# Optimization experiments

Measured on AMD Instinct MI355X. Metric: run time of the kernel, lower is better.

## Reference

```python
import jax, jax.numpy as jnp
import numpy as np

B, NS, NI, UP = 1024, 64, 64, 4
H = 256


def setup_inputs() -> dict:
    key = jax.random.key(0)
    ks = list(jax.random.split(key, 40))
    it = iter(ks)
    def lin(din, dout):
        return (jax.random.normal(next(it), (din, dout), jnp.float32) / np.sqrt(din)).astype(jnp.float32)
    d = {}
    d['rays_o'] = jax.random.normal(next(it), (B, 3), jnp.float32) * 0.1
    rd = jax.random.normal(next(it), (B, 3), jnp.float32)
    d['rays_d'] = rd / jnp.linalg.norm(rd, axis=-1, keepdims=True)
    d['near'] = jnp.full((B, 1), 0.5, jnp.float32)
    d['far'] = jnp.full((B, 1), 2.5, jnp.float32)
    d['W_sdf0'] = lin(3, H); d['b_sdf0'] = jnp.zeros((H,), jnp.float32)
    d['W_sdf1'] = lin(H, H); d['b_sdf1'] = jnp.zeros((H,), jnp.float32)
    d['W_sdf2'] = lin(H, 1 + H); d['b_sdf2'] = jnp.zeros((1 + H,), jnp.float32)
    d['s_var'] = jnp.asarray(0.3, jnp.float32)
    d['Wc0'] = lin(9 + H, H); d['bc0'] = jnp.zeros((H,), jnp.float32)
    d['Wc1'] = lin(H, 3); d['bc1'] = jnp.zeros((3,), jnp.float32)
    d['Wn0'] = lin(6, H); d['bn0'] = jnp.zeros((H,), jnp.float32)
    d['Wn1'] = lin(H, H); d['bn1'] = jnp.zeros((H,), jnp.float32)
    d['Wn2'] = lin(H, 4); d['bn2'] = jnp.zeros((4,), jnp.float32)
    d['Wrf0'] = lin(3, H); d['brf0'] = jnp.zeros((H,), jnp.float32)
    d['Wrf1'] = lin(H, 1); d['brf1'] = jnp.zeros((1,), jnp.float32)
    d['Wrl0'] = lin(3, H); d['brl0'] = jnp.zeros((H,), jnp.float32)
    d['Wrl1'] = lin(H, 1); d['brl1'] = jnp.zeros((1,), jnp.float32)
    d['Wnm0'] = lin(H, 128); d['bnm0'] = jnp.zeros((128,), jnp.float32)
    d['Wnm1'] = lin(128, 3); d['bnm1'] = jnp.zeros((3,), jnp.float32)
    return d


def _forward(args):
    (rays_o, rays_d, near, far, W_sdf0, b_sdf0, W_sdf1, b_sdf1, W_sdf2, b_sdf2,
     s_var, Wc0, bc0, Wc1, bc1, Wn0, bn0, Wn1, bn1, Wn2, bn2,
     Wrf0, brf0, Wrf1, brf1, Wrl0, brl0, Wrl1, brl1, Wnm0, bnm0, Wnm1, bnm1) = args
    relu, sig = jax.nn.relu, jax.nn.sigmoid
    Bn = rays_o.shape[0]
    inv_s = jnp.clip(jnp.exp(10.0 * s_var), 1e-6, 1e6)  # SingleVarianceNetwork
    sample_dist = 2.0 / NS

    def sdf_out(p):
        h = relu(p @ W_sdf0 + b_sdf0)
        h = relu(h @ W_sdf1 + b_sdf1)
        return h @ W_sdf2 + b_sdf2  # [N, 1+256]: sdf + feature

    def sdf_val(p):
        return sdf_out(p)[..., 0]

    def sample_pdf(bins, weights, n):  # deterministic (perturb=False)
        w = weights + 1e-5
        pdf = w / jnp.sum(w, -1, keepdims=True)
        cdf = jnp.concatenate([jnp.zeros_like(pdf[:, :1]), jnp.cumsum(pdf, -1)], -1)
        u = jnp.broadcast_to(jnp.linspace(0.5 / n, 1.0 - 0.5 / n, n, dtype=bins.dtype), (bins.shape[0], n))
        inds = jax.vmap(lambda c, uu: jnp.searchsorted(c, uu, side='right'))(cdf, u)
        below = jnp.clip(inds - 1, 0, bins.shape[-1] - 1)
        above = jnp.clip(inds, 0, bins.shape[-1] - 1)
        cb = jnp.take_along_axis(cdf, below, -1); ca = jnp.take_along_axis(cdf, above, -1)
        bb = jnp.take_along_axis(bins, below, -1); ba = jnp.take_along_axis(bins, above, -1)
        denom = jnp.where(ca - cb < 1e-5, 1.0, ca - cb)
        return bb + (u - cb) / denom * (ba - bb)

    def up_sample(o, d, z, sdf, n_imp, s):  # NeuS hierarchical SDF upsampling
        pts = o[:, None, :] + d[:, None, :] * z[..., None]
        radius = jnp.linalg.norm(pts, axis=-1)
        inside = ((radius[:, :-1] < 1.0) | (radius[:, 1:] < 1.0)).astype(z.dtype)
        prev_sdf, next_sdf = sdf[:, :-1], sdf[:, 1:]
        prev_z, next_z = z[:, :-1], z[:, 1:]
        mid_sdf = 0.5 * (prev_sdf + next_sdf)
        cos_val = (next_sdf - prev_sdf) / (next_z - prev_z + 1e-5)
        prev_cos = jnp.concatenate([jnp.zeros_like(cos_val[:, :1]), cos_val[:, :-1]], -1)
        cos_val = jnp.clip(jnp.minimum(cos_val, prev_cos), -1e3, 0.0) * inside
        dist = next_z - prev_z
        pc = sig((mid_sdf - 0.5 * cos_val * dist) * s)
        nc = sig((mid_sdf + 0.5 * cos_val * dist) * s)
        alpha = (pc - nc + 1e-5) / (pc + 1e-5)
        trans = jnp.cumprod(jnp.concatenate([jnp.ones_like(alpha[:, :1]), 1.0 - alpha + 1e-7], -1), -1)[:, :-1]
        return sample_pdf(z, alpha * trans, n_imp)

    def importance_sdf(o, d):
        z = near + (far - near) * jnp.linspace(0.0, 1.0, NS)[None, :]
        sdf = sdf_val((o[:, None, :] + d[:, None, :] * z[..., None]).reshape(-1, 3)).reshape(Bn, -1)
        for i in range(UP):
            nz = up_sample(o, d, z, sdf, NI // UP, 64.0 * 2 ** i)
            z = jnp.sort(jnp.concatenate([z, nz], -1), -1)
            if i + 1 < UP:
                sdf = sdf_val((o[:, None, :] + d[:, None, :] * z[..., None]).reshape(-1, 3)).reshape(Bn, -1)
        return jax.lax.stop_gradient(z)  # sampler runs under no_grad

    def render_sdf(o, d, z):  # rendering_rays_SDF (NeuS)
        S = z.shape[1]
        dists = jnp.concatenate([z[:, 1:] - z[:, :-1], jnp.full_like(z[:, :1], sample_dist)], -1)
        mid_z = z + 0.5 * dists
        pts = (o[:, None, :] + d[:, None, :] * mid_z[..., None]).reshape(-1, 3)
        dirs = jnp.broadcast_to(d[:, None, :], (Bn, S, 3)).reshape(-1, 3)
        out = sdf_out(pts)
        sdf = out[:, :1]; feat = out[:, 1:]
        grads = jax.grad(lambda p: jnp.sum(sdf_val(p)))(pts)  # analytic SDF gradient
        true_cos = jnp.sum(dirs * grads, -1, keepdims=True)
        iter_cos = -relu(-true_cos)  # cos_anneal_ratio = 1.0
        df = dists.reshape(-1, 1)
        pc = sig((sdf - 0.5 * iter_cos * df) * inv_s)
        nc = sig((sdf + 0.5 * iter_cos * df) * inv_s)
        alpha = jnp.clip((pc - nc + 1e-5) / (pc + 1e-5), 0.0, 1.0).reshape(Bn, S)
        trans = jnp.cumprod(jnp.concatenate([jnp.ones_like(alpha[:, :1]), 1.0 - alpha + 1e-7], -1), -1)[:, :-1]
        w = alpha * trans
        depths = jax.lax.stop_gradient(jnp.sum(mid_z * w, -1, keepdims=True))  # AlphaBlend depth, no_grad
        nrm = grads / (jnp.linalg.norm(grads, axis=-1, keepdims=True) + 1e-12)  # NormalizedAnalytic
        cin = jnp.concatenate([pts, nrm, dirs, feat], -1)  # color_d_in=9 + 256 feat
        rgb = sig(relu(cin @ Wc0 + bc0) @ Wc1 + bc1).reshape(Bn, S, 3)
        color = jnp.sum(rgb * w[..., None], 1)
        smooth = ((feat @ Wnm0 + bnm0) @ Wnm1 + bnm1).reshape(Bn, S, 3)  # Linear->Linear, no act
        surf_n = jnp.sum(w[..., None] * nrm.reshape(Bn, S, 3), 1)
        surf_n = surf_n / (jnp.linalg.norm(surf_n, axis=-1, keepdims=True) + 1e-12)
        return color, w, depths, surf_n, smooth

    def nerf_eval(pts, dirs):
        h = relu(jnp.concatenate([pts, dirs], -1) @ Wn0 + bn0)
        h = relu(h @ Wn1 + bn1)
        o = h @ Wn2 + bn2
        return o[:, 0], sig(o[:, 1:4])

    def mask_prob(pts, Wa, ba, Wb, bb):  # Refract/ReflectNetwork, d_in=3 d_out=1
        return sig((relu(pts @ Wa + ba) @ Wb + bb)[:, 0])

    def importance_nerf(o, d, z, n_imp):
        S = z.shape[1]
        dists = jnp.concatenate([z[:, 1:] - z[:, :-1], jnp.full_like(z[:, :1], 1e10)], -1)
        pts = (o[:, None, :] + d[:, None, :] * z[..., None]).reshape(-1, 3)
        dirs = jnp.broadcast_to(d[:, None, :], (Bn, S, 3)).reshape(-1, 3)
        sigma, _ = nerf_eval(pts, dirs)
        alpha = 1.0 - jnp.exp(-relu(sigma).reshape(Bn, S) * dists)
        trans = jnp.cumprod(jnp.concatenate([jnp.ones_like(alpha[:, :1]), 1.0 - alpha + 1e-7], -1), -1)[:, :-1]
        w = alpha * trans
        nz = sample_pdf(z, w[:, :-1], n_imp)
        return jax.lax.stop_gradient(jnp.sort(jnp.concatenate([z, nz], -1), -1))

    def render_nerf(o, d, z):
        S = z.shape[1]
        dists = jnp.concatenate([z[:, 1:] - z[:, :-1], jnp.full_like(z[:, :1], sample_dist)], -1)
        mid_z = z + 0.5 * dists
        pts = (o[:, None, :] + d[:, None, :] * mid_z[..., None]).reshape(-1, 3)
        dirs = jnp.broadcast_to(d[:, None, :], (Bn, S, 3)).reshape(-1, 3)
        sigma, rgb = nerf_eval(pts, dirs)
        alpha = 1.0 - jnp.exp(-relu(sigma).reshape(Bn, S) * dists)
        trans = jnp.cumprod(jnp.concatenate([jnp.ones_like(alpha[:, :1]), 1.0 - alpha + 1e-7], -1), -1)[:, :-1]
        w = alpha * trans
        color = jnp.sum(rgb.reshape(Bn, S, 3) * w[..., None], 1)
        m1 = jnp.sum(w * mask_prob(pts, Wrf0, brf0, Wrf1, brf1).reshape(Bn, S), -1, keepdims=True)
        m2 = jnp.sum(w * mask_prob(pts, Wrl0, brl0, Wrl1, brl1).reshape(Bn, S), -1, keepdims=True)
        return color, m1, m2

    # ---- main pipeline (eval: perturb=False, geometry_warmup_state=False) ----
    z_sdf = importance_sdf(rays_o, rays_d)
    _color_sdf, _w_sdf, depths, surf_n, _smooth = render_sdf(rays_o, rays_d, z_sdf)

    z0 = near + (far - near) * jnp.linspace(0.0, 1.0, NS)[None, :]
    z1 = importance_nerf(rays_o, rays_d, z0, NI)
    c1, m1, m2 = render_nerf(rays_o, rays_d, z1)

    # hit point + reflect/refract directions
    hit = rays_o + rays_d * depths
    n = surf_n
    cos = jnp.sum(rays_d * n, -1, keepdims=True)
    n = jnp.where(cos > 0, -n, n)  # face the incoming ray
    cosi = -jnp.sum(rays_d * n, -1, keepdims=True)
    refl = rays_d + 2.0 * cosi * n
    eta = 1.0 / 1.5
    k = 1.0 - eta * eta * (1.0 - cosi * cosi)
    refr = eta * rays_d + (eta * cosi - jnp.sqrt(jnp.maximum(k, 0.0))) * n
    refr = jnp.where(k < 0, refl, refr)  # total internal reflection
    refl = refl / (jnp.linalg.norm(refl, axis=-1, keepdims=True) + 1e-12)
    refr = refr / (jnp.linalg.norm(refr, axis=-1, keepdims=True) + 1e-12)

    ones = jnp.ones((Bn, 1), z1.dtype)
    # reflect (fanshe) pass: near=0.05 far=3.7
    zf0 = 0.05 * ones + (3.7 - 0.05) * jnp.linspace(0.0, 1.0, NS)[None, :]
    zf = importance_nerf(hit, refl, zf0, NI)
    cf, _, _ = render_nerf(hit, refl, zf)
    # refract (zheshe) passes: (0,3.7) and (0.5,3.7) with half samples
    zz0 = 3.7 * jnp.linspace(0.0, 1.0, NS // 2)[None, :] * ones
    zz = importance_nerf(hit, refr, zz0, NI // 2)
    cz, _, _ = render_nerf(hit, refr, zz)
    zb0 = 0.5 * ones + (3.7 - 0.5) * jnp.linspace(0.0, 1.0, NS // 2)[None, :]
    zb = importance_nerf(hit, refr, zb0, NI // 2)
    cb_, _, _ = render_nerf(hit, refr, zb)
    rgb_z = 0.5 * cz + 0.5 * cb_

    rgb = c1 * (1.0 - m2) + cf * m2
    rgb = rgb * (1.0 - m1) + rgb_z * m1
    return rgb


def reference(rays_o, rays_d, near, far, W_sdf0, b_sdf0, W_sdf1, b_sdf1, W_sdf2, b_sdf2,
              s_var, Wc0, bc0, Wc1, bc1, Wn0, bn0, Wn1, bn1, Wn2, bn2,
              Wrf0, brf0, Wrf1, brf1, Wrl0, brl0, Wrl1, brl1, Wnm0, bnm0, Wnm1, bnm1):
    return _forward((rays_o, rays_d, near, far, W_sdf0, b_sdf0, W_sdf1, b_sdf1, W_sdf2, b_sdf2,
                     s_var, Wc0, bc0, Wc1, bc1, Wn0, bn0, Wn1, bn1, Wn2, bn2,
                     Wrf0, brf0, Wrf1, brf1, Wrl0, brl0, Wrl1, brl1, Wnm0, bnm0, Wnm1, bnm1))
```

## Files before the change

### kernel.cpp

```cpp
#include <hip/hip_runtime.h>

#define NB 1024
#define HH 256
#define ZS 128
#define PP 16
#define SAMPLE_DIST 0.03125f

typedef __attribute__((ext_vector_type(8))) _Float16 half8v;
typedef __attribute__((ext_vector_type(4))) float f32x4;

struct ZInit { int on; const float* loA; const float* hiA; float lo0,hi0,lo1,hi1; };

__device__ __forceinline__ float sigm(float x){ return 1.0f/(1.0f+__expf(-x)); }

__device__ __forceinline__ void gload_lds16(const void* g, void* l){
  __builtin_amdgcn_global_load_lds(
      (const __attribute__((address_space(1))) unsigned int*)g,
      (__attribute__((address_space(3))) unsigned int*)l, 16, 0, 0);
}

__device__ __forceinline__ float iscan_prod(float v, int lane){
  #pragma unroll
  for (int o=1;o<64;o<<=1){ float u=__shfl_up(v,o); if(lane>=o) v*=u; }
  return v;
}
__device__ __forceinline__ float iscan_sum(float v, int lane){
  #pragma unroll
  for (int o=1;o<64;o<<=1){ float u=__shfl_up(v,o); if(lane>=o) v+=u; }
  return v;
}
__device__ __forceinline__ float wave_sum(float v){
  #pragma unroll
  for (int o=1;o<64;o<<=1) v += __shfl_xor(v,o);
  return v;
}

__device__ __forceinline__ void load_point2(const float* __restrict__ o, const float* __restrict__ dv,
    const float* __restrict__ z, int idx, int S, int midflag, int zst, ZInit zi, float* pt, float* dir)
{
  int r = idx / S;
  int i = idx - r*S;
  float zz;
  if (zi.on){
    float a=zi.loA[r], b=zi.hiA[r];
    zz = a + (b-a)*((float)i/(float)(S-1));
    if (midflag){
      float z1 = a + (b-a)*((float)(i+1)/(float)(S-1));
      zz = (i < S-1) ? 0.5f*(zz+z1) : (zz + 0.5f*SAMPLE_DIST);
    }
  } else {
    const float* zr = z + r*zst;
    zz = zr[i];
    if (midflag) zz = (i < S-1) ? 0.5f*(zz + zr[i+1]) : (zz + 0.5f*SAMPLE_DIST);
  }
  #pragma unroll
  for (int c=0;c<3;c++){
    float dc = dv[r*3+c];
    pt[c] = o[r*3+c] + dc*zz;
    if (dir) dir[c] = dc;
  }
}

__device__ __forceinline__ void load_point(const float* __restrict__ o, const float* __restrict__ dv,
    const float* __restrict__ z, int idx, int S, int midflag, float* pt, float* dir)
{
  int r = idx / S;
  int i = idx - r*S;
  const float* zr = z + r*ZS;
  float zz = zr[i];
  if (midflag) zz = (i < S-1) ? 0.5f*(zz + zr[i+1]) : (zz + 0.5f*SAMPLE_DIST);
  #pragma unroll
  for (int c=0;c<3;c++){
    float dc = dv[r*3+c];
    pt[c] = o[r*3+c] + dc*zz;
    if (dir) dir[c] = dc;
  }
}

__global__ __launch_bounds__(256) void prep_kernel(const float* __restrict__ W1, const float* __restrict__ W2,
    float* __restrict__ W1T, float* __restrict__ w2col)
{
  int idx = blockIdx.x*256 + threadIdx.x;
  int j = idx >> 8, k = idx & 255;
  W1T[j*HH + k] = W1[k*HH + j];
  if (idx < HH) w2col[idx] = W2[idx*257];
}

__global__ __launch_bounds__(256) void prep_bfrag_kernel(const float* __restrict__ W1,
    short* __restrict__ Bh)
{
  int idx = blockIdx.x*256 + threadIdx.x;
  int j = idx & 7;
  int lane = (idx>>3) & 63;
  int s = (idx>>9) & 7;
  int nt = idx >> 12;
  int k = s*32 + ((lane>>4)<<3) + j;
  int n = nt*16 + (lane&15);
  union { _Float16 h; short s; } u;
  u.h = (_Float16)W1[k*256 + n];
  Bh[idx] = u.s;
}

__global__ void build_rays_kernel(const float* __restrict__ ro, const float* __restrict__ rd,
    const float* __restrict__ nearA, const float* __restrict__ farA,
    const float* __restrict__ hit, const float* __restrict__ refl, const float* __restrict__ refr,
    float* __restrict__ rO, float* __restrict__ rD, float* __restrict__ rLo, float* __restrict__ rHi)
{
  int r = blockIdx.x*256 + threadIdx.x;
  if (r >= 4096) return;
  int m = r>>10, q = r&1023;
  const float* so; const float* sd; float lo,hi;
  if (m==0){ so=ro+q*3; sd=rd+q*3; lo=nearA[q]; hi=farA[q]; }
  else if (m==1){ so=hit+q*3; sd=refl+q*3; lo=0.05f; hi=3.7f; }
  else if (m==2){ so=hit+q*3; sd=refr+q*3; lo=0.f; hi=3.7f; }
  else { so=hit+q*3; sd=refr+q*3; lo=0.5f; hi=3.7f; }
  rO[r*3]=so[0]; rO[r*3+1]=so[1]; rO[r*3+2]=so[2];
  rD[r*3]=sd[0]; rD[r*3+1]=sd[1]; rD[r*3+2]=sd[2];
  rLo[r]=lo; rHi[r]=hi;
}

__global__ __launch_bounds__(256) void sdf_mfma_kernel(
    const float* __restrict__ o, const float* __restrict__ dv, const float* __restrict__ z,
    int S, int midflag, int zst, ZInit zi,
    const float* __restrict__ W0, const float* __restrict__ b0,
    const short* __restrict__ Bh, const float* __restrict__ b1,
    const float* __restrict__ w2col, const float* __restrict__ b2,
    float* __restrict__ out_sdf, unsigned short* __restrict__ signs)
{
  __shared__ short ldsB[2][8192];
  __shared__ float xs[128][5];
  __shared__ float w0s[3*HH];
  __shared__ float b0s[HH];
  int t = threadIdx.x;
  int base = blockIdx.x*128;
  int wave=t>>6, lane=t&63, g=lane>>4, c16=lane&15;
  for (int i=t;i<3*HH;i+=256) w0s[i]=W0[i];
  b0s[t]=b0[t];
  if (t<128){
    float pt[3];
    load_point2(o,dv,z,base+t,S,midflag,zst,zi,pt,nullptr);
    xs[t][0]=pt[0]; xs[t][1]=pt[1]; xs[t][2]=pt[2];
  }
  {
    const char* gb = (const char*)Bh;
    #pragma unroll
    for (int c=0;c<4;c++){
      int ch = wave*4 + c;
      gload_lds16(gb + ch*1024 + lane*16, (void*)&ldsB[0][ch*512]);
    }
  }
  __syncthreads();
  half8v af[2][8];
  #pragma unroll
  for (int mt=0;mt<2;mt++){
    const float* xp = xs[wave*32 + mt*16 + c16];
    float x0=xp[0],x1=xp[1],x2=xp[2];
    #pragma unroll
    for (int s8=0;s8<8;s8++){
      int nb = s8*32 + g*8;
      union { _Float16 h[8]; half8v v; } uh;
      #pragma unroll
      for (int j=0;j<8;j++){
        int n=nb+j;
        float a=b0s[n];
        a=fmaf(x0,w0s[n],a);
        a=fmaf(x1,w0s[HH+n],a);
        a=fmaf(x2,w0s[2*HH+n],a);
        uh.h[j]=(_Float16)fmaxf(a,0.f);
      }
      af[mt][s8]=uh.v;
    }
  }
  float pacc[2][4];
  #pragma unroll
  for (int mt=0;mt<2;mt++){ pacc[mt][0]=0.f; pacc[mt][1]=0.f; pacc[mt][2]=0.f; pacc[mt][3]=0.f; }
  int buf=0;
  for (int ntp=0;ntp<8;ntp++){
    if (ntp<7){
      const char* gb = (const char*)(Bh + 2*(ntp+1)*4096);
      #pragma unroll
      for (int c=0;c<4;c++){
        int ch = wave*4 + c;
        gload_lds16(gb + ch*1024 + lane*16, (void*)&ldsB[buf^1][ch*512]);
      }
    }
    int nt0=2*ntp;
    f32x4 aH[2][2];
    #pragma unroll
    for (int mt=0;mt<2;mt++)
      #pragma unroll
      for (int h=0;h<2;h++) aH[mt][h]=(f32x4){0.f,0.f,0.f,0.f};
    const short* Lb = &ldsB[buf][0];
    #pragma unroll
    for (int s8=0;s8<8;s8++){
      half8v bh0 = *(const half8v*)(Lb + s8*512 + lane*8);
      half8v bh1 = *(const half8v*)(Lb + 4096 + s8*512 + lane*8);
      #pragma unroll
      for (int mt=0;mt<2;mt++){
        aH[mt][0] = __builtin_amdgcn_mfma_f32_16x16x32_f16(af[mt][s8], bh0, aH[mt][0], 0,0,0);
        aH[mt][1] = __builtin_amdgcn_mfma_f32_16x16x32_f16(af[mt][s8], bh1, aH[mt][1], 0,0,0);
      }
    }
    #pragma unroll
    for (int h=0;h<2;h++){
      int nt = nt0+h;
      int n = nt*16 + c16;
      float b1v = b1[n];
      float wv = w2col[n];
      #pragma unroll
      for (int mt=0;mt<2;mt++){
        f32x4 acc = aH[mt][h];
        #pragma unroll
        for (int rr=0;rr<4;rr++){
          float hv = acc[rr]+b1v;
          if (signs){
            unsigned long long m0 = __ballot(hv>0.f);
            if (c16==0) signs[(base+wave*32+mt*16+g*4+rr)*16+nt] = (unsigned short)(m0>>(16*g));
          }
          pacc[mt][rr]=fmaf(fmaxf(hv,0.f),wv,pacc[mt][rr]);
        }
      }
    }
    __syncthreads();
    buf^=1;
  }
  #pragma unroll
  for (int mt=0;mt<2;mt++)
    #pragma unroll
    for (int rr=0;rr<4;rr++){
      float v=pacc[mt][rr];
      v+=__shfl_xor(v,1); v+=__shfl_xor(v,2); v+=__shfl_xor(v,4); v+=__shfl_xor(v,8);
      pacc[mt][rr]=v;
    }
  if (c16==0){
    float bb2=b2[0];
    #pragma unroll
    for (int mt=0;mt<2;mt++)
      #pragma unroll
      for (int rr=0;rr<4;rr++)
        out_sdf[base + wave*32 + mt*16 + g*4 + rr] = pacc[mt][rr] + bb2;
  }
}

__global__ __launch_bounds__(256) void sdf_bwd_mfma_kernel(
    const float* __restrict__ o, const float* __restrict__ dv, const float* __restrict__ z,
    const float* __restrict__ W0, const float* __restrict__ b0,
    const unsigned short* __restrict__ signs,
    const short* __restrict__ Th,
    const float* __restrict__ w2col,
    float* __restrict__ out_grad)
{
  __shared__ short ldsB[2][8192];
  __shared__ float xs[128][5];
  __shared__ float w0s[3*HH];
  __shared__ float b0s[HH];
  __shared__ _Float16 w2h_s[HH];
  int t = threadIdx.x;
  int base = blockIdx.x*128;
  int wave=t>>6, lane=t&63, g=lane>>4, c16=lane&15;
  for (int i=t;i<3*HH;i+=256) w0s[i]=W0[i];
  b0s[t]=b0[t];
  w2h_s[t]=(_Float16)w2col[t];
  if (t<128){
    float pt[3];
    ZInit zn{0,nullptr,nullptr,0,0,0,0};
    load_point2(o,dv,z,base+t,128,1,ZS,zn,pt,nullptr);
    xs[t][0]=pt[0]; xs[t][1]=pt[1]; xs[t][2]=pt[2];
  }
  {
    const char* gb = (const char*)Th;
    #pragma unroll
    for (int c=0;c<4;c++){
      int ch = wave*4 + c;
      gload_lds16(gb + ch*1024 + lane*16, (void*)&ldsB[0][ch*512]);
    }
  }
  __syncthreads();
  half8v af[2][8];
  #pragma unroll
  for (int mt=0;mt<2;mt++){
    int ptA = base + wave*32 + mt*16 + c16;
    #pragma unroll
    for (int s8=0;s8<8;s8++){
      int j0 = s8*32 + g*8;
      unsigned short wch = signs[ptA*16 + (j0>>4)];
      unsigned bits = ((unsigned)wch >> ((g&1)*8)) & 0xFFu;
      union { _Float16 h[8]; half8v v; } uh;
      #pragma unroll
      for (int jj=0;jj<8;jj++){
        bool on = (bits>>jj)&1u;
        uh.h[jj] = on ? w2h_s[j0+jj] : (_Float16)0.f;
      }
      af[mt][s8]=uh.v;
    }
  }
  float acc3[2][4][3];
  #pragma unroll
  for (int mt=0;mt<2;mt++)
    #pragma unroll
    for (int rr=0;rr<4;rr++){ acc3[mt][rr][0]=0.f; acc3[mt][rr][1]=0.f; acc3[mt][rr][2]=0.f; }
  int buf=0;
  for (int ntp=0;ntp<8;ntp++){
    if (ntp<7){
      const char* gb = (const char*)(Th + 2*(ntp+1)*4096);
      #pragma unroll
      for (int c=0;c<4;c++){
        int ch = wave*4 + c;
        gload_lds16(gb + ch*1024 + lane*16, (void*)&ldsB[buf^1][ch*512]);
      }
    }
    int nt0=2*ntp;
    f32x4 aH[2][2];
    #pragma unroll
    for (int mt=0;mt<2;mt++)
      #pragma unroll
      for (int h=0;h<2;h++) aH[mt][h]=(f32x4){0.f,0.f,0.f,0.f};
    const short* Lb = &ldsB[buf][0];
    #pragma unroll
    for (int s8=0;s8<8;s8++){
      half8v bh0 = *(const half8v*)(Lb + s8*512 + lane*8);
      half8v bh1 = *(const half8v*)(Lb + 4096 + s8*512 + lane*8);
      #pragma unroll
      for (int mt=0;mt<2;mt++){
        aH[mt][0] = __builtin_amdgcn_mfma_f32_16x16x32_f16(af[mt][s8], bh0, aH[mt][0], 0,0,0);
        aH[mt][1] = __builtin_amdgcn_mfma_f32_16x16x32_f16(af[mt][s8], bh1, aH[mt][1], 0,0,0);
      }
    }
    #pragma unroll
    for (int h=0;h<2;h++){
      int nt = nt0+h;
      int tn = nt*16 + c16;
      float w0a=w0s[tn], w0b=w0s[HH+tn], w0c=w0s[2*HH+tn], bb=b0s[tn];
      #pragma unroll
      for (int mt=0;mt<2;mt++){
        f32x4 acc = aH[mt][h];
        #pragma unroll
        for (int rr=0;rr<4;rr++){
          const float* xq = xs[wave*32 + mt*16 + g*4 + rr];
          float h0 = fmaf(xq[0],w0a, fmaf(xq[1],w0b, fmaf(xq[2],w0c, bb)));
          float dh0 = (h0>0.f) ? acc[rr] : 0.f;
          acc3[mt][rr][0]=fmaf(dh0,w0a,acc3[mt][rr][0]);
          acc3[mt][rr][1]=fmaf(dh0,w0b,acc3[mt][rr][1]);
          acc3[mt][rr][2]=fmaf(dh0,w0c,acc3[mt][rr][2]);
        }
      }
    }
    __syncthreads();
    buf^=1;
  }
  #pragma unroll
  for (int mt=0;mt<2;mt++)
    #pragma unroll
    for (int rr=0;rr<4;rr++)
      #pragma unroll
      for (int cc=0;cc<3;cc++){
        float v=acc3[mt][rr][cc];
        v+=__shfl_xor(v,1); v+=__shfl_xor(v,2); v+=__shfl_xor(v,4); v+=__shfl_xor(v,8);
        acc3[mt][rr][cc]=v;
      }
  if (c16==0){
    #pragma unroll
    for (int mt=0;mt<2;mt++)
      #pragma unroll
      for (int rr=0;rr<4;rr++){
        int pt_ = base + wave*32 + mt*16 + g*4 + rr;
        out_grad[pt_*3+0]=acc3[mt][rr][0];
        out_grad[pt_*3+1]=acc3[mt][rr][1];
        out_grad[pt_*3+2]=acc3[mt][rr][2];
      }
  }
}

__global__ __launch_bounds__(256) void nerf_mfma_batch(
    const float* __restrict__ rO, const float* __restrict__ rD,
    const float* __restrict__ rLo, const float* __restrict__ rHi,
    const float* __restrict__ zbuf, int ptsA, int lgSA, int lgSB, int NRA, int useZ, int midflag,
    const float* __restrict__ W0, const float* __restrict__ b0,
    const short* __restrict__ Bh, const float* __restrict__ b1,
    const float* __restrict__ W2, const float* __restrict__ b2,
    float* __restrict__ out_sigma, float* __restrict__ out_rgb)
{
  __shared__ short ldsB[2][8192];
  __shared__ float w0s[6*HH];
  __shared__ float b0s[HH];
  int t = threadIdx.x;
  int base = blockIdx.x*128;
  int wave=t>>6, lane=t&63, g=lane>>4, c16=lane&15;
  for (int i=t;i<6*HH;i+=256) w0s[i]=W0[i];
  b0s[t]=b0[t];
  {
    const char* gb = (const char*)Bh;
    #pragma unroll
    for (int c=0;c<4;c++){
      int ch = wave*4 + c;
      gload_lds16(gb + ch*1024 + lane*16, (void*)&ldsB[0][ch*512]);
    }
  }
  float xv[2][6];
  #pragma unroll
  for (int mt=0;mt<2;mt++){
    int idx = base + wave*32 + mt*16 + c16;
    int r,i,S;
    if (idx<ptsA){ r=idx>>lgSA; i=idx-(r<<lgSA); S=1<<lgSA; }
    else { int q=idx-ptsA; int rq=q>>lgSB; r=NRA+rq; i=q-(rq<<lgSB); S=1<<lgSB; }
    float zz;
    if (!useZ){
      float a=rLo[r], b=rHi[r];
      zz = a + (b-a)*((float)i/(float)(S-1));
      if (midflag){
        float z1 = a + (b-a)*((float)(i+1)/(float)(S-1));
        zz = (i<S-1)? 0.5f*(zz+z1) : (zz+0.5f*SAMPLE_DIST);
      }
    } else {
      const float* zr = zbuf + r*128;
      zz = zr[i];
      if (midflag) zz = (i<S-1)? 0.5f*(zz+zr[i+1]) : (zz+0.5f*SAMPLE_DIST);
    }
    #pragma unroll
    for (int c=0;c<3;c++){
      float dc=rD[r*3+c];
      xv[mt][c]   = rO[r*3+c] + dc*zz;
      xv[mt][3+c] = dc;
    }
  }
  __syncthreads();
  half8v af[2][8];
  #pragma unroll
  for (int mt=0;mt<2;mt++){
    float x0=xv[mt][0],x1=xv[mt][1],x2=xv[mt][2],x3=xv[mt][3],x4=xv[mt][4],x5=xv[mt][5];
    #pragma unroll
    for (int s8=0;s8<8;s8++){
      int nb = s8*32 + g*8;
      union { _Float16 h[8]; half8v v; } uh;
      #pragma unroll
      for (int j=0;j<8;j++){
        int n=nb+j;
        float a=b0s[n];
        a=fmaf(x0,w0s[n],a);
        a=fmaf(x1,w0s[HH+n],a);
        a=fmaf(x2,w0s[2*HH+n],a);
        a=fmaf(x3,w0s[3*HH+n],a);
        a=fmaf(x4,w0s[4*HH+n],a);
        a=fmaf(x5,w0s[5*HH+n],a);
        uh.h[j]=(_Float16)fmaxf(a,0.f);
      }
      af[mt][s8]=uh.v;
    }
  }
  float pacc[2][4][4];
  #pragma unroll
  for (int mt=0;mt<2;mt++)
    #pragma unroll
    for (int rr=0;rr<4;rr++){ pacc[mt][rr][0]=0.f; pacc[mt][rr][1]=0.f; pacc[mt][rr][2]=0.f; pacc[mt][rr][3]=0.f; }
  int buf=0;
  for (int ntp=0;ntp<8;ntp++){
    if (ntp<7){
      const char* gb = (const char*)(Bh + 2*(ntp+1)*4096);
      #pragma unroll
      for (int c=0;c<4;c++){
        int ch = wave*4 + c;
        gload_lds16(gb + ch*1024 + lane*16, (void*)&ldsB[buf^1][ch*512]);
      }
    }
    int nt0=2*ntp;
    f32x4 aH[2][2];
    #pragma unroll
    for (int mt=0;mt<2;mt++)
      #pragma unroll
      for (int h=0;h<2;h++) aH[mt][h]=(f32x4){0.f,0.f,0.f,0.f};
    const short* Lb = &ldsB[buf][0];
    #pragma unroll
    for (int s8=0;s8<8;s8++){
      half8v bh0 = *(const half8v*)(Lb + s8*512 + lane*8);
      half8v bh1 = *(const half8v*)(Lb + 4096 + s8*512 + lane*8);
      #pragma unroll
      for (int mt=0;mt<2;mt++){
        aH[mt][0] = __builtin_amdgcn_mfma_f32_16x16x32_f16(af[mt][s8], bh0, aH[mt][0], 0,0,0);
        aH[mt][1] = __builtin_amdgcn_mfma_f32_16x16x32_f16(af[mt][s8], bh1, aH[mt][1], 0,0,0);
      }
    }
    #pragma unroll
    for (int h=0;h<2;h++){
      int nt = nt0+h;
      int n = nt*16 + c16;
      float b1v = b1[n];
      float4 w2v = *(const float4*)(W2 + n*4);
      #pragma unroll
      for (int mt=0;mt<2;mt++){
        f32x4 acc = aH[mt][h];
        #pragma unroll
        for (int rr=0;rr<4;rr++){
          float hh = fmaxf(acc[rr]+b1v, 0.f);
          pacc[mt][rr][0]=fmaf(hh,w2v.x,pacc[mt][rr][0]);
          pacc[mt][rr][1]=fmaf(hh,w2v.y,pacc[mt][rr][1]);
          pacc[mt][rr][2]=fmaf(hh,w2v.z,pacc[mt][rr][2]);
          pacc[mt][rr][3]=fmaf(hh,w2v.w,pacc[mt][rr][3]);
        }
      }
    }
    __syncthreads();
    buf^=1;
  }
  #pragma unroll
  for (int mt=0;mt<2;mt++)
    #pragma unroll
    for (int rr=0;rr<4;rr++)
      #pragma unroll
      for (int c=0;c<4;c++){
        float v=pacc[mt][rr][c];
        v+=__shfl_xor(v,1); v+=__shfl_xor(v,2); v+=__shfl_xor(v,4); v+=__shfl_xor(v,8);
        pacc[mt][rr][c]=v;
      }
  if (c16==0){
    float bb0=b2[0], bb1=b2[1], bb2v=b2[2], bb3=b2[3];
    #pragma unroll
    for (int mt=0;mt<2;mt++)
      #pragma unroll
      for (int rr=0;rr<4;rr++){
        int pt_ = base + wave*32 + mt*16 + g*4 + rr;
        out_sigma[pt_] = pacc[mt][rr][0] + bb0;
        out_rgb[pt_*3+0] = sigm(pacc[mt][rr][1] + bb1);
        out_rgb[pt_*3+1] = sigm(pacc[mt][rr][2] + bb2v);
        out_rgb[pt_*3+2] = sigm(pacc[mt][rr][3] + bb3);
      }
  }
}

__global__ __launch_bounds__(256) void mask_kernel(
    const float* __restrict__ o, const float* __restrict__ dv, const float* __restrict__ z, int S,
    const float* __restrict__ Wa0, const float* __restrict__ ba0, const float* __restrict__ Wa1, const float* __restrict__ ba1,
    const float* __restrict__ Wb0, const float* __restrict__ bb0, const float* __restrict__ Wb1, const float* __restrict__ bb1,
    float* __restrict__ outA, float* __restrict__ outB)
{
  __shared__ __align__(16) float hA[PP][HH];
  __shared__ float pin[PP][4];
  __shared__ float part[PP][16];
  int t=threadIdx.x;
  int base=blockIdx.x*PP;
  if (t<PP){
    float pt[3];
    load_point(o,dv,z,base+t,S,1,pt,nullptr);
    pin[t][0]=pt[0]; pin[t][1]=pt[1]; pin[t][2]=pt[2];
  }
  __syncthreads();
  {
    float w0=Wa0[t], w1=Wa0[HH+t], w2=Wa0[2*HH+t], bb=ba0[t];
    #pragma unroll
    for (int p=0;p<PP;p++){
      float v = fmaf(pin[p][0],w0, fmaf(pin[p][1],w1, fmaf(pin[p][2],w2, bb)));
      hA[p][t]=fmaxf(v,0.f);
    }
  }
  __syncthreads();
  {
    int p=t>>4, g=t&15;
    float s=0.f;
    #pragma unroll
    for (int m=0;m<16;m++){ int j=g+16*m; s=fmaf(hA[p][j], Wa1[j], s); }
    part[p][g]=s;
  }
  __syncthreads();
  if (t<PP){
    float s=ba1[0];
    #pragma unroll
    for (int g=0;g<16;g++) s+=part[t][g];
    outA[base+t]=sigm(s);
  }
  __syncthreads();
  {
    float w0=Wb0[t], w1=Wb0[HH+t], w2=Wb0[2*HH+t], bb=bb0[t];
    #pragma unroll
    for (int p=0;p<PP;p++){
      float v = fmaf(pin[p][0],w0, fmaf(pin[p][1],w1, fmaf(pin[p][2],w2, bb)));
      hA[p][t]=fmaxf(v,0.f);
    }
  }
  __syncthreads();
  {
    int p=t>>4, g=t&15;
    float s=0.f;
    #pragma unroll
    for (int m=0;m<16;m++){ int j=g+16*m; s=fmaf(hA[p][j], Wb1[j], s); }
    part[p][g]=s;
  }
  __syncthreads();
  if (t<PP){
    float s=bb1[0];
    #pragma unroll
    for (int g=0;g<16;g++) s+=part[t][g];
    outB[base+t]=sigm(s);
  }
}

__global__ __launch_bounds__(256) void upsample_wave_kernel(float* __restrict__ z,
    const float* __restrict__ sdf, const float* __restrict__ o, const float* __restrict__ dv,
    int S, float s, ZInit zi)
{
  __shared__ float zsh[4][128], ssh[4][128], csh[4][128], nzsh[4][16];
  int wave=threadIdx.x>>6, lane=threadIdx.x&63;
  int r=blockIdx.x*4+wave;
  float* zs=zsh[wave]; float* ss=ssh[wave]; float* cs=csh[wave]; float* nzs=nzsh[wave];
  for (int i=lane;i<S;i+=64){
    float zv;
    if (zi.on){
      float a=zi.loA[r], b=zi.hiA[r];
      zv = a + (b-a)*((float)i/(float)(S-1));
    } else zv = z[r*ZS+i];
    zs[i]=zv; ss[i]=sdf[r*S+i];
  }
  __syncthreads();
  float ox=o[r*3],oy=o[r*3+1],oz=o[r*3+2];
  float dx=dv[r*3],dy=dv[r*3+1],dz=dv[r*3+2];
  int M=S-1;
  auto alpha_at=[&](int k)->float{
    float z0=zs[k], z1=zs[k+1], s0=ss[k], s1=ss[k+1];
    float craw=(s1-s0)/(z1-z0+1e-5f);
    float cprev=(k>0)? (ss[k]-ss[k-1])/(zs[k]-zs[k-1]+1e-5f) : 0.f;
    float cv=fminf(craw,cprev);
    cv=fminf(fmaxf(cv,-1000.f),0.f);
    float px=ox+dx*z0, py=oy+dy*z0, pz=oz+dz*z0;
    float qx=ox+dx*z1, qy=oy+dy*z1, qz=oz+dz*z1;
    float r0=sqrtf(px*px+py*py+pz*pz);
    float r1=sqrtf(qx*qx+qy*qy+qz*qz);
    float inside=(r0<1.f||r1<1.f)?1.f:0.f;
    cv*=inside;
    float mid=0.5f*(s0+s1), dist=z1-z0;
    float pc=sigm((mid-0.5f*cv*dist)*s);
    float nc=sigm((mid+0.5f*cv*dist)*s);
    return (pc-nc+1e-5f)/(pc+1e-5f);
  };
  float al0=(lane<M)? alpha_at(lane):0.f;
  float al1=(lane+64<M)? alpha_at(lane+64):0.f;
  float f0=(lane<M)?(1.f-al0+1e-7f):1.f;
  float f1=(lane+64<M)?(1.f-al1+1e-7f):1.f;
  float ip0=iscan_prod(f0,lane);
  float tt=__shfl_up(ip0,1); float T0=(lane==0)?1.f:tt;
  float tot0=__shfl(ip0,63);
  float ip1=iscan_prod(f1,lane);
  float tu=__shfl_up(ip1,1); float T1=((lane==0)?1.f:tu)*tot0;
  float w0=(lane<M)? al0*T0+1e-5f:0.f;
  float w1=(lane+64<M)? al1*T1+1e-5f:0.f;
  float wsum=wave_sum(w0+w1);
  float inv=1.f/wsum;
  float is0=iscan_sum(w0,lane);
  float st0=__shfl(is0,63);
  float is1=iscan_sum(w1,lane)+st0;
  if (lane<M) cs[lane+1]=is0*inv;
  if (lane+64<M) cs[lane+64+1]=is1*inv;
  if (lane==0) cs[0]=0.f;
  __syncthreads();
  if (lane<16){
    float u=(lane+0.5f)/16.f;
    int lo=0,hi=S;
    while(lo<hi){ int m=(lo+hi)>>1; if(cs[m]<=u) lo=m+1; else hi=m; }
    int below=lo-1; below=below<0?0:(below>S-1?S-1:below);
    int above=lo>S-1?S-1:lo;
    float cb=cs[below], ca=cs[above], bb=zs[below], ba=zs[above];
    float dd=ca-cb; float den=(dd<1e-5f)?1.f:dd;
    nzs[lane]=bb+(u-cb)/den*(ba-bb);
  }
  __syncthreads();
  for (int i=lane;i<S;i+=64){
    float zi_=zs[i]; int cnt=0;
    #pragma unroll
    for (int j=0;j<16;j++) cnt += (nzs[j]<zi_)?1:0;
    z[r*ZS+i+cnt]=zi_;
  }
  if (lane<16){
    float v=nzs[lane]; int rk=0;
    #pragma unroll
    for (int j=0;j<16;j++) rk += ((nzs[j]<v)||(nzs[j]==v&&j<lane))?1:0;
    int lo=0,hi=S;
    while(lo<hi){ int m=(lo+hi)>>1; if(zs[m]<=v) lo=m+1; else hi=m; }
    z[r*ZS+lo+rk]=v;
  }
}

__global__ __launch_bounds__(256) void nerf_imp_batch(float* __restrict__ zbuf,
    const float* __restrict__ sigma, const float* __restrict__ rLo, const float* __restrict__ rHi,
    int ptsA, int NRA)
{
  __shared__ float zsh[4][64], csh[4][64], nzsh[4][64];
  int wave=threadIdx.x>>6, lane=threadIdx.x&63;
  int r=blockIdx.x*4+wave;
  int S = (r<NRA)? 64 : 32;
  int n = S;
  int off = (r<NRA)? r*64 : ptsA + (r-NRA)*32;
  float* zs=zsh[wave]; float* cs=csh[wave]; float* nzs=nzsh[wave];
  if (lane<S){
    float a=rLo[r], b=rHi[r];
    zs[lane]= a + (b-a)*((float)lane/(float)(S-1));
  }
  __syncthreads();
  int M=S-1;
  float al=0.f;
  if (lane<M){
    float d_=zs[lane+1]-zs[lane];
    float sv=sigma[off+lane];
    al=1.f-__expf(-fmaxf(sv,0.f)*d_);
  }
  float f=(lane<M)?(1.f-al+1e-7f):1.f;
  float ip=iscan_prod(f,lane);
  float tt=__shfl_up(ip,1); float T=(lane==0)?1.f:tt;
  float w=(lane<M)? al*T+1e-5f:0.f;
  float wsum=wave_sum(w);
  float inv=1.f/wsum;
  float is=iscan_sum(w,lane);
  if (lane<M) cs[lane+1]=is*inv;
  if (lane==0) cs[0]=0.f;
  __syncthreads();
  if (lane<n){
    float u=(lane+0.5f)/(float)n;
    int lo=0,hi=S;
    while(lo<hi){ int m=(lo+hi)>>1; if(cs[m]<=u) lo=m+1; else hi=m; }
    int below=lo-1; below=below<0?0:(below>S-1?S-1:below);
    int above=lo>S-1?S-1:lo;
    float cb=cs[below], ca=cs[above], bb=zs[below], ba=zs[above];
    float dd=ca-cb; float den=(dd<1e-5f)?1.f:dd;
    nzs[lane]=bb+(u-cb)/den*(ba-bb);
  }
  __syncthreads();
  if (lane<S){
    float zi_=zs[lane]; int cnt=0;
    for (int j=0;j<n;j++) cnt += (nzs[j]<zi_)?1:0;
    zbuf[r*128+lane+cnt]=zi_;
  }
  if (lane<n){
    float v=nzs[lane]; int rk=0;
    for (int j=0;j<n;j++) rk += ((nzs[j]<v)||(nzs[j]==v&&j<lane))?1:0;
    int lo=0,hi=S;
    while(lo<hi){ int m=(lo+hi)>>1; if(zs[m]<=v) lo=m+1; else hi=m; }
    zbuf[r*128+lo+rk]=v;
  }
}

__global__ __launch_bounds__(256) void nerf_render_batch(const float* __restrict__ zbuf,
    const float* __restrict__ sigma, const float* __restrict__ rgbp,
    int pts2A, int NRA,
    const float* __restrict__ mva, const float* __restrict__ mvb,
    float* __restrict__ c1b, float* __restrict__ m1b, float* __restrict__ m2b,
    float* __restrict__ cfb, float* __restrict__ czb, float* __restrict__ cbb)
{
  int wave=threadIdx.x>>6, lane=threadIdx.x&63;
  int r=blockIdx.x*4+wave;
  int S = (r<NRA)? 128 : 64;
  int off = (r<NRA)? r*128 : pts2A + (r-NRA)*64;
  const float* zr = zbuf + r*128;
  int domask = (r<1024);
  float a0=0.f,a1=0.f;
  if (lane<S){
    float d_=(lane<S-1)? zr[lane+1]-zr[lane] : SAMPLE_DIST;
    a0=1.f-__expf(-fmaxf(sigma[off+lane],0.f)*d_);
  }
  if (lane+64<S){
    int k=lane+64;
    float d_=(k<S-1)? zr[k+1]-zr[k] : SAMPLE_DIST;
    a1=1.f-__expf(-fmaxf(sigma[off+k],0.f)*d_);
  }
  float f0=(lane<S)?(1.f-a0+1e-7f):1.f;
  float f1=(lane+64<S)?(1.f-a1+1e-7f):1.f;
  float ip0=iscan_prod(f0,lane);
  float tt=__shfl_up(ip0,1); float T0=(lane==0)?1.f:tt;
  float tot0=__shfl(ip0,63);
  float ip1=iscan_prod(f1,lane);
  float tu=__shfl_up(ip1,1); float T1=((lane==0)?1.f:tu)*tot0;
  float w0=(lane<S)? a0*T0:0.f;
  float w1=(lane+64<S)? a1*T1:0.f;
  float c0=0,c1=0,c2=0,m1=0,m2=0;
  if (lane<S){
    int i0=off+lane;
    c0=w0*rgbp[i0*3]; c1=w0*rgbp[i0*3+1]; c2=w0*rgbp[i0*3+2];
    if (domask){ m1=w0*mva[i0]; m2=w0*mvb[i0]; }
  }
  if (lane+64<S){
    int i1=off+lane+64;
    c0=fmaf(w1,rgbp[i1*3],c0); c1=fmaf(w1,rgbp[i1*3+1],c1); c2=fmaf(w1,rgbp[i1*3+2],c2);
    if (domask){ m1=fmaf(w1,mva[i1],m1); m2=fmaf(w1,mvb[i1],m2); }
  }
  c0=wave_sum(c0); c1=wave_sum(c1); c2=wave_sum(c2);
  m1=wave_sum(m1); m2=wave_sum(m2);
  if (lane==0){
    int grp=r>>10, q=r&1023;
    float* outc = (grp==0)? c1b : (grp==1)? cfb : (grp==2)? czb : cbb;
    outc[q*3]=c0; outc[q*3+1]=c1; outc[q*3+2]=c2;
    if (grp==0){ m1b[q]=m1; m2b[q]=m2; }
  }
}

__global__ __launch_bounds__(256) void sdf_render_hit(const float* __restrict__ z,
    const float* __restrict__ sdf, const float* __restrict__ grad,
    const float* __restrict__ o, const float* __restrict__ dv,
    const float* __restrict__ svar,
    float* __restrict__ hitb, float* __restrict__ reflb, float* __restrict__ refrb)
{
  int wave=threadIdx.x>>6, lane=threadIdx.x&63;
  int r=blockIdx.x*4+wave;
  float inv_s=fminf(fmaxf(__expf(10.f*svar[0]),1e-6f),1e6f);
  float dx=dv[r*3],dy=dv[r*3+1],dz=dv[r*3+2];
  const float* zr=z+r*ZS;
  auto comp=[&](int k, float& alpha, float& midz, float& gx, float& gy, float& gz){
    float d_=(k<127)? zr[k+1]-zr[k] : SAMPLE_DIST;
    midz=zr[k]+0.5f*d_;
    int gi=(r*128+k)*3;
    gx=grad[gi]; gy=grad[gi+1]; gz=grad[gi+2];
    float tc=dx*gx+dy*gy+dz*gz;
    float ic=fminf(tc,0.f);
    float s_=sdf[r*128+k];
    float pc=sigm((s_-0.5f*ic*d_)*inv_s);
    float nc=sigm((s_+0.5f*ic*d_)*inv_s);
    alpha=fminf(fmaxf((pc-nc+1e-5f)/(pc+1e-5f),0.f),1.f);
  };
  float al0,mz0,g0x,g0y,g0z; comp(lane,al0,mz0,g0x,g0y,g0z);
  float al1,mz1,g1x,g1y,g1z; comp(lane+64,al1,mz1,g1x,g1y,g1z);
  float f0=1.f-al0+1e-7f, f1=1.f-al1+1e-7f;
  float ip0=iscan_prod(f0,lane);
  float tt=__shfl_up(ip0,1); float T0=(lane==0)?1.f:tt;
  float tot0=__shfl(ip0,63);
  float ip1=iscan_prod(f1,lane);
  float tu=__shfl_up(ip1,1); float T1=((lane==0)?1.f:tu)*tot0;
  float w0=al0*T0, w1=al1*T1;
  float n0=1.f/(sqrtf(g0x*g0x+g0y*g0y+g0z*g0z)+1e-12f);
  float n1=1.f/(sqrtf(g1x*g1x+g1y*g1y+g1z*g1z)+1e-12f);
  float dep=w0*mz0+w1*mz1;
  float sx=w0*n0*g0x+w1*n1*g1x;
  float sy=w0*n0*g0y+w1*n1*g1y;
  float sz=w0*n0*g0z+w1*n1*g1z;
  dep=wave_sum(dep); sx=wave_sum(sx); sy=wave_sum(sy); sz=wave_sum(sz);
  if (lane==0){
    float nn=1.f/(sqrtf(sx*sx+sy*sy+sz*sz)+1e-12f);
    float nx=sx*nn, ny=sy*nn, nz=sz*nn;
    hitb[r*3]  = o[r*3]  +dx*dep;
    hitb[r*3+1]= o[r*3+1]+dy*dep;
    hitb[r*3+2]= o[r*3+2]+dz*dep;
    float cs=dx*nx+dy*ny+dz*nz;
    if (cs>0.f){ nx=-nx; ny=-ny; nz=-nz; }
    float cosi=-(dx*nx+dy*ny+dz*nz);
    float rx=dx+2.f*cosi*nx, ry=dy+2.f*cosi*ny, rz=dz+2.f*cosi*nz;
    float eta=1.f/1.5f;
    float k=1.f-eta*eta*(1.f-cosi*cosi);
    float sq=sqrtf(fmaxf(k,0.f));
    float tx=eta*dx+(eta*cosi-sq)*nx;
    float ty=eta*dy+(eta*cosi-sq)*ny;
    float tz=eta*dz+(eta*cosi-sq)*nz;
    if (k<0.f){ tx=rx; ty=ry; tz=rz; }
    float rn=1.f/(sqrtf(rx*rx+ry*ry+rz*rz)+1e-12f);
    reflb[r*3]=rx*rn; reflb[r*3+1]=ry*rn; reflb[r*3+2]=rz*rn;
    float tn=1.f/(sqrtf(tx*tx+ty*ty+tz*tz)+1e-12f);
    refrb[r*3]=tx*tn; refrb[r*3+1]=ty*tn; refrb[r*3+2]=tz*tn;
  }
}

__global__ void compose_kernel(const float* __restrict__ c1b, const float* __restrict__ m1b,
    const float* __restrict__ m2b, const float* __restrict__ cfb, const float* __restrict__ czb,
    const float* __restrict__ cbb, float* __restrict__ out)
{
  int r = blockIdx.x*blockDim.x + threadIdx.x;
  if (r >= NB) return;
  float m1=m1b[r], m2=m2b[r];
  #pragma unroll
  for (int c=0;c<3;c++){
    float v = c1b[r*3+c]*(1.f-m2) + cfb[r*3+c]*m2;
    float rz = 0.5f*czb[r*3+c] + 0.5f*cbb[r*3+c];
    out[r*3+c] = v*(1.f-m1) + rz*m1;
  }
}

extern "C" void kernel_launch(void* const* d_in, const int* in_sizes, int n_in,
                              void* d_out, int out_size, void* d_ws, size_t ws_size,
                              hipStream_t stream)
{
  const float* rays_o=(const float*)d_in[0];
  const float* rays_d=(const float*)d_in[1];
  const float* nearA =(const float*)d_in[2];
  const float* farA  =(const float*)d_in[3];
  const float* Ws0=(const float*)d_in[4];
  const float* bs0=(const float*)d_in[5];
  const float* Ws1=(const float*)d_in[6];
  const float* bs1=(const float*)d_in[7];
  const float* Ws2=(const float*)d_in[8];
  const float* bs2=(const float*)d_in[9];
  const float* svar=(const float*)d_in[10];
  const float* Wn0=(const float*)d_in[15];
  const float* bn0=(const float*)d_in[16];
  const float* Wn1=(const float*)d_in[17];
  const float* bn1=(const float*)d_in[18];
  const float* Wn2=(const float*)d_in[19];
  const float* bn2=(const float*)d_in[20];
  const float* Wrf0=(const float*)d_in[21];
  const float* brf0=(const float*)d_in[22];
  const float* Wrf1=(const float*)d_in[23];
  const float* brf1=(const float*)d_in[24];
  const float* Wrl0=(const float*)d_in[25];
  const float* brl0=(const float*)d_in[26];
  const float* Wrl1=(const float*)d_in[27];
  const float* brl1=(const float*)d_in[28];

  const int NRA   = 2048;
  const int PTS1A = 2048*64;
  const int PTS2A = 2048*128;

  float* ws=(float*)d_ws;
  float* zbuf = ws;  ws += 4096*128;
  float* sdfb = ws;  ws += 393216;
  float* uni  = ws;  ws += 1441792;
  float* gradb = uni;
  unsigned short* signsb = (unsigned short*)(uni + 393216);
  float* rgbp = uni;
  float* mv1  = ws;  ws += PTS1A;
  float* mv2  = ws;  ws += PTS1A;
  float* W1T  = ws;  ws += HH*HH;
  float* w2c  = ws;  ws += HH;
  float* rO   = ws;  ws += 4096*3;
  float* rD   = ws;  ws += 4096*3;
  float* rLo  = ws;  ws += 4096;
  float* rHi  = ws;  ws += 4096;
  float* hitb = ws;  ws += NB*3;
  float* reflb= ws;  ws += NB*3;
  float* refrb= ws;  ws += NB*3;
  float* c1b  = ws;  ws += NB*3;
  float* m1b  = ws;  ws += NB;
  float* m2b  = ws;  ws += NB;
  float* cfb  = ws;  ws += NB*3;
  float* czb  = ws;  ws += NB*3;
  float* cbb  = ws;  ws += NB*3;
  short* bfragN = (short*)ws; ws += HH*HH/2;
  short* bfragS = (short*)ws; ws += HH*HH/2;
  short* bfragT = (short*)ws; ws += HH*HH/2;

  const int RB = (NB+255)/256;
  const int WB = NB/4;

  ZInit ziNone{0,nullptr,nullptr,0.f,0.f,0.f,0.f};
  ZInit ziNF  {1,nearA,farA,0.f,0.f,0.f,0.f};

  prep_kernel<<<256,256,0,stream>>>(Ws1, Ws2, W1T, w2c);
  prep_bfrag_kernel<<<256,256,0,stream>>>(Wn1, bfragN);
  prep_bfrag_kernel<<<256,256,0,stream>>>(Ws1, bfragS);
  prep_bfrag_kernel<<<256,256,0,stream>>>(W1T, bfragT);

  for (int i=0;i<4;i++){
    int S=64+16*i;
    float sscale=64.f*(float)(1<<i);
    sdf_mfma_kernel<<<NB*S/128,256,0,stream>>>(rays_o,rays_d,zbuf,S,0,ZS,(i==0?ziNF:ziNone),
        Ws0,bs0, bfragS,bs1, w2c,bs2, sdfb, nullptr);
    upsample_wave_kernel<<<WB,256,0,stream>>>(zbuf,sdfb,rays_o,rays_d,S,sscale,(i==0?ziNF:ziNone));
  }

  sdf_mfma_kernel<<<NB*128/128,256,0,stream>>>(rays_o,rays_d,zbuf,128,1,ZS,ziNone,
      Ws0,bs0, bfragS,bs1, w2c,bs2, sdfb, signsb);
  sdf_bwd_mfma_kernel<<<NB*128/128,256,0,stream>>>(rays_o,rays_d,zbuf, Ws0,bs0, signsb,
      bfragT, w2c, gradb);
  sdf_render_hit<<<WB,256,0,stream>>>(zbuf,sdfb,gradb,rays_o,rays_d,svar, hitb,reflb,refrb);

  build_rays_kernel<<<16,256,0,stream>>>(rays_o,rays_d,nearA,farA, hitb,reflb,refrb, rO,rD,rLo,rHi);

  nerf_mfma_batch<<<(PTS1A + 2048*32)/128,256,0,stream>>>(rO,rD,rLo,rHi, zbuf,
      PTS1A, 6, 5, NRA, 0, 0,
      Wn0,bn0, bfragN,bn1, Wn2,bn2, sdfb,rgbp);
  nerf_imp_batch<<<4096/4,256,0,stream>>>(zbuf, sdfb, rLo,rHi, PTS1A, NRA);
  nerf_mfma_batch<<<(PTS2A + 2048*64)/128,256,0,stream>>>(rO,rD,rLo,rHi, zbuf,
      PTS2A, 7, 6, NRA, 1, 1,
      Wn0,bn0, bfragN,bn1, Wn2,bn2, sdfb,rgbp);
  mask_kernel<<<NB*128/PP,256,0,stream>>>(rays_o,rays_d,zbuf,128, Wrf0,brf0,Wrf1,brf1, Wrl0,brl0,Wrl1,brl1, mv1,mv2);
  nerf_render_batch<<<4096/4,256,0,stream>>>(zbuf, sdfb, rgbp, PTS2A, NRA, mv1,mv2,
      c1b,m1b,m2b, cfb,czb,cbb);

  compose_kernel<<<RB,256,0,stream>>>(c1b,m1b,m2b,cfb,czb,cbb,(float*)d_out);
}
```

Measured before the change: 391.1 us.

## Compute NeRF first layer with MFMA using a prepacked fp16 weight fragment

Replaces the scalar FMA evaluation of the NeRF first layer (6 inputs plus bias, 256 outputs) with MFMA 16x16x32 instructions. The bias is folded in as a constant-one input column. A new prep kernel packs W0 and b0 into A-fragment order, and the layer-1 B fragments are re-permuted ('rho' layout) so that the MFMA output registers can feed the next MFMA directly as A operands. This removes the per-block LDS staging of fp32 W0 and many VALU FMAs, at the cost of fp16 rounding of the inputs and weights, an extra barrier, and reuse of the second LDS buffer.

After: 375.6 us. 4.0% less time.

```diff
diff --git a/kernel.cpp b/kernel.cpp
--- a/kernel.cpp
+++ b/kernel.cpp
@@ -99,6 +99,39 @@
   union { _Float16 h; short s; } u;
   u.h = (_Float16)W1[k*256 + n];
   Bh[idx] = u.s;
+}
+
+__global__ __launch_bounds__(256) void prep_bfrag_rho_kernel(const float* __restrict__ W1,
+    short* __restrict__ Bh)
+{
+  int idx = blockIdx.x*256 + threadIdx.x;
+  int j = idx & 7;
+  int lane = (idx>>3) & 63;
+  int s = (idx>>9) & 7;
+  int nt = idx >> 12;
+  int g = lane>>4;
+  int k = 32*s + 16*(j>>2) + 4*g + (j&3);
+  int n = nt*16 + (lane&15);
+  union { _Float16 h; short s; } u;
+  u.h = (_Float16)W1[k*256 + n];
+  Bh[idx] = u.s;
+}
+
+__global__ __launch_bounds__(256) void prep_a0_kernel(const float* __restrict__ W0,
+    const float* __restrict__ b0, short* __restrict__ A0h)
+{
+  int idx = blockIdx.x*256 + threadIdx.x;
+  if (idx >= 8192) return;
+  int j = idx & 7;
+  int lane = (idx>>3) & 63;
+  int m = idx >> 9;
+  int g = lane>>4, row = lane&15;
+  int k = g*8 + j;
+  int n0 = m*16 + row;
+  float v = (k<6) ? W0[k*256 + n0] : (k==6 ? b0[n0] : 0.f);
+  union { _Float16 h; short s; } u;
+  u.h = (_Float16)v;
+  A0h[idx] = u.s;
 }
 
 __global__ void build_rays_kernel(const float* __restrict__ ro, const float* __restrict__ rd,
@@ -375,24 +408,21 @@
     const float* __restrict__ rO, const float* __restrict__ rD,
     const float* __restrict__ rLo, const float* __restrict__ rHi,
     const float* __restrict__ zbuf, int ptsA, int lgSA, int lgSB, int NRA, int useZ, int midflag,
-    const float* __restrict__ W0, const float* __restrict__ b0,
-    const short* __restrict__ Bh, const float* __restrict__ b1,
+    const short* __restrict__ A0h, const short* __restrict__ Bh, const float* __restrict__ b1,
     const float* __restrict__ W2, const float* __restrict__ b2,
     float* __restrict__ out_sigma, float* __restrict__ out_rgb)
 {
   __shared__ short ldsB[2][8192];
-  __shared__ float w0s[6*HH];
-  __shared__ float b0s[HH];
   int t = threadIdx.x;
   int base = blockIdx.x*128;
   int wave=t>>6, lane=t&63, g=lane>>4, c16=lane&15;
-  for (int i=t;i<6*HH;i+=256) w0s[i]=W0[i];
-  b0s[t]=b0[t];
   {
+    const char* ga = (const char*)A0h;
     const char* gb = (const char*)Bh;
     #pragma unroll
     for (int c=0;c<4;c++){
       int ch = wave*4 + c;
+      gload_lds16(ga + ch*1024 + lane*16, (void*)&ldsB[1][ch*512]);
       gload_lds16(gb + ch*1024 + lane*16, (void*)&ldsB[0][ch*512]);
     }
   }
@@ -423,30 +453,37 @@
       xv[mt][3+c] = dc;
     }
   }
+  half8v bx[2];
+  #pragma unroll
+  for (int mt=0;mt<2;mt++){
+    union { _Float16 h[8]; half8v v; } u;
+    #pragma unroll
+    for (int c=0;c<6;c++) u.h[c]=(_Float16)xv[mt][c];
+    u.h[6]=(_Float16)1.f; u.h[7]=(_Float16)0.f;
+    bx[mt]=u.v;
+  }
   __syncthreads();
   half8v af[2][8];
   #pragma unroll
-  for (int mt=0;mt<2;mt++){
-    float x0=xv[mt][0],x1=xv[mt][1],x2=xv[mt][2],x3=xv[mt][3],x4=xv[mt][4],x5=xv[mt][5];
-    #pragma unroll
-    for (int s8=0;s8<8;s8++){
-      int nb = s8*32 + g*8;
-      union { _Float16 h[8]; half8v v; } uh;
-      #pragma unroll
-      for (int j=0;j<8;j++){
-        int n=nb+j;
-        float a=b0s[n];
-        a=fmaf(x0,w0s[n],a);
-        a=fmaf(x1,w0s[HH+n],a);
-        a=fmaf(x2,w0s[2*HH+n],a);
-        a=fmaf(x3,w0s[3*HH+n],a);
-        a=fmaf(x4,w0s[4*HH+n],a);
-        a=fmaf(x5,w0s[5*HH+n],a);
-        uh.h[j]=(_Float16)fmaxf(a,0.f);
-      }
-      af[mt][s8]=uh.v;
-    }
-  }
+  for (int s8=0;s8<8;s8++){
+    half8v a0a = *(const half8v*)&ldsB[1][(2*s8)*512 + lane*8];
+    half8v a0b = *(const half8v*)&ldsB[1][(2*s8+1)*512 + lane*8];
+    f32x4 z4 = (f32x4){0.f,0.f,0.f,0.f};
+    f32x4 da0 = __builtin_amdgcn_mfma_f32_16x16x32_f16(a0a, bx[0], z4, 0,0,0);
+    f32x4 da1 = __builtin_amdgcn_mfma_f32_16x16x32_f16(a0a, bx[1], z4, 0,0,0);
+    f32x4 db0 = __builtin_amdgcn_mfma_f32_16x16x32_f16(a0b, bx[0], z4, 0,0,0);
+    f32x4 db1 = __builtin_amdgcn_mfma_f32_16x16x32_f16(a0b, bx[1], z4, 0,0,0);
+    union { _Float16 h[8]; half8v v; } u0, u1;
+    #pragma unroll
+    for (int rr=0;rr<4;rr++){
+      u0.h[rr]   = (_Float16)fmaxf(da0[rr],0.f);
+      u0.h[4+rr] = (_Float16)fmaxf(db0[rr],0.f);
+      u1.h[rr]   = (_Float16)fmaxf(da1[rr],0.f);
+      u1.h[4+rr] = (_Float16)fmaxf(db1[rr],0.f);
+    }
+    af[0][s8]=u0.v; af[1][s8]=u1.v;
+  }
+  __syncthreads();
   float pacc[2][4][4];
   #pragma unroll
   for (int mt=0;mt<2;mt++)
@@ -926,6 +963,7 @@
   short* bfragN = (short*)ws; ws += HH*HH/2;
   short* bfragS = (short*)ws; ws += HH*HH/2;
   short* bfragT = (short*)ws; ws += HH*HH/2;
+  short* a0N    = (short*)ws; ws += 4096;
 
   const int RB = (NB+255)/256;
   const int WB = NB/4;
@@ -934,9 +972,10 @@
   ZInit ziNF  {1,nearA,farA,0.f,0.f,0.f,0.f};
 
   prep_kernel<<<256,256,0,stream>>>(Ws1, Ws2, W1T, w2c);
-  prep_bfrag_kernel<<<256,256,0,stream>>>(Wn1, bfragN);
+  prep_bfrag_rho_kernel<<<256,256,0,stream>>>(Wn1, bfragN);
   prep_bfrag_kernel<<<256,256,0,stream>>>(Ws1, bfragS);
   prep_bfrag_kernel<<<256,256,0,stream>>>(W1T, bfragT);
+  prep_a0_kernel<<<32,256,0,stream>>>(Wn0, bn0, a0N);
 
   for (int i=0;i<4;i++){
     int S=64+16*i;
@@ -956,11 +995,11 @@
 
   nerf_mfma_batch<<<(PTS1A + 2048*32)/128,256,0,stream>>>(rO,rD,rLo,rHi, zbuf,
       PTS1A, 6, 5, NRA, 0, 0,
-      Wn0,bn0, bfragN,bn1, Wn2,bn2, sdfb,rgbp);
+      a0N, bfragN, bn1, Wn2,bn2, sdfb,rgbp);
   nerf_imp_batch<<<4096/4,256,0,stream>>>(zbuf, sdfb, rLo,rHi, PTS1A, NRA);
   nerf_mfma_batch<<<(PTS2A + 2048*64)/128,256,0,stream>>>(rO,rD,rLo,rHi, zbuf,
       PTS2A, 7, 6, NRA, 1, 1,
-      Wn0,bn0, bfragN,bn1, Wn2,bn2, sdfb,rgbp);
+      a0N, bfragN, bn1, Wn2,bn2, sdfb,rgbp);
   mask_kernel<<<NB*128/PP,256,0,stream>>>(rays_o,rays_d,zbuf,128, Wrf0,brf0,Wrf1,brf1, Wrl0,brl0,Wrl1,brl1, mv1,mv2);
   nerf_render_batch<<<4096/4,256,0,stream>>>(zbuf, sdfb, rgbp, PTS2A, NRA, mv1,mv2,
       c1b,m1b,m2b, cfb,czb,cbb);
```
